# Kernel optimization log

Measured on AMD Instinct MI355X. Metric: run time of the kernel, lower is better.

## Reference

```python
import jax, jax.numpy as jnp
import numpy as np

B, C, H, W, K = 64, 64, 32, 32, 1024  # C == dim_dict, K == size_dict
BETA = 0.25


def setup_inputs() -> dict:
    key = jax.random.key(0)
    k1, k2, k3 = jax.random.split(key, 3)
    return {
        "z_from_encoder": jax.random.normal(k1, (B, C, H, W), dtype=jnp.float32),
        "codebook": jax.random.normal(k2, (K, C), dtype=jnp.float32),
        "codebook_weight": jax.random.normal(k3, (K,), dtype=jnp.float32),
        "flg_train": 1,
    }


def reference(z_from_encoder, codebook, codebook_weight, flg_train):
    # NCHW -> NHWC, flatten to (N, D)
    z = jnp.transpose(z_from_encoder, (0, 2, 3, 1))
    zf = z.reshape(-1, z.shape[-1])                      # (N, D)
    # squared euclidean distances via expansion (N, K)
    d = (jnp.sum(zf ** 2, axis=1, keepdims=True)
         + jnp.sum(codebook ** 2, axis=1)
         - 2.0 * zf @ codebook.T)
    idx = jnp.argmin(d, axis=1)                          # (N,)
    # one-hot @ codebook == gather
    z_q = codebook[idx].reshape(z.shape)                 # (B, H, W, D)
    if flg_train:
        loss = (BETA * jnp.mean((jax.lax.stop_gradient(z_q) - z) ** 2)
                + jnp.mean((z_q - jax.lax.stop_gradient(z)) ** 2))
    else:
        loss = jnp.float32(0.0)
    # straight-through estimator
    z_q_st = z + jax.lax.stop_gradient(z_q - z)
    # codebook usage histogram -> perplexity
    n_tok = zf.shape[0]
    e_mean = jnp.zeros((codebook.shape[0],), z.dtype).at[idx].add(1.0) / n_tok
    perplexity = jnp.exp(-jnp.sum(e_mean * jnp.log(e_mean + 1e-10)))
    z_q_out = jnp.transpose(z_q_st, (0, 3, 1, 2))        # back to NCHW
    return z_q_out, loss, perplexity
```

## Files before the change

kernel.cpp:

```cpp
#include <hip/hip_runtime.h>


typedef __attribute__((ext_vector_type(8))) short short8;
typedef __attribute__((ext_vector_type(4))) float float4v;

#define NELEM 4194304

#define WS_CBF   0
#define WS_C2H   262144
#define WS_HIST  266240
#define WS_LOSS  270336
#define WS_IDX   270592

__device__ __forceinline__ unsigned bf16_rne(float x) {
    unsigned u = __float_as_uint(x);
    return (u + 0x7fffu + ((u >> 16) & 1u)) >> 16;
}

__global__ __launch_bounds__(256) void prep_kernel(
    const float* __restrict__ cb, ushort* __restrict__ cbf,
    float* __restrict__ c2h, int* __restrict__ hist, float* __restrict__ loss_part) {
    __shared__ float s_c2[2][16];
    int tid  = threadIdx.x;
    int lane = tid & 63, wave = tid >> 6;
    int quad = lane >> 4, col = lane & 15;
    int bx   = blockIdx.x;

    if (bx >= 64) {
        hist[(bx - 64) * 256 + tid] = 0;
        if (bx == 64 && tid < 64) loss_part[tid] = 0.f;
        return;
    }
    int c = bx, fid = wave;
    int st = fid & 1, split = fid >> 1;
    int code  = c * 16 + col;
    int dbase = st * 32 + quad * 8;
    const float* cp = cb + code * 64 + dbase;
    float4v v0 = *(const float4v*)cp;
    float4v v1 = *(const float4v*)(cp + 4);
    float xs[8] = {v0.x, v0.y, v0.z, v0.w, v1.x, v1.y, v1.z, v1.w};
    short8 frag;
    float ssq = 0.f;
#pragma unroll
    for (int j = 0; j < 8; j++) {
        float x = xs[j];
        ssq = fmaf(x, x, ssq);
        unsigned hb = bf16_rne(x);
        if (split == 0) frag[j] = (short)hb;
        else            frag[j] = (short)bf16_rne(x - __uint_as_float(hb << 16));
    }
    *(short8*)(cbf + ((c * 4 + fid) * 64 + lane) * 8) = frag;
    if (split == 0) {
        ssq += __shfl_xor(ssq, 16);
        ssq += __shfl_xor(ssq, 32);
        if (quad == 0) s_c2[st][col] = ssq;
    }
    __syncthreads();
    if (tid < 16) c2h[c * 16 + tid] = -0.5f * (s_c2[0][tid] + s_c2[1][tid]);
}

__global__ __launch_bounds__(256, 3) void argmin_kernel(
    const float* __restrict__ z, const ushort* __restrict__ cbf,
    const float* __restrict__ c2h, int* __restrict__ idx_out, int* __restrict__ hist)
{
    __shared__ float s_ms[4][64];
    __shared__ int   s_mi[4][64];

    int tid  = threadIdx.x;
    int lane = tid & 63, wave = tid >> 6;
    int quad = lane >> 4, col = lane & 15;
    int bx   = blockIdx.x;

    int tokbase = bx * 64;
    int bb = tokbase >> 10, hwb = tokbase & 1023;
    const float* zb = z + bb * 65536 + hwb;

    short8 ah[4][2], al[4][2];
#pragma unroll
    for (int g = 0; g < 4; g++) {
        int rel = g * 16 + col;
#pragma unroll
        for (int st = 0; st < 2; st++) {
            short8 h8, l8;
#pragma unroll
            for (int j = 0; j < 8; j++) {
                int d = st * 32 + quad * 8 + j;
                float x = zb[d * 1024 + rel];
                unsigned hb = bf16_rne(x);
                h8[j] = (short)hb;
                l8[j] = (short)bf16_rne(x - __uint_as_float(hb << 16));
            }
            ah[g][st] = h8; al[g][st] = l8;
        }
    }

    float best[4][4]; int bidx[4][4];
#pragma unroll
    for (int g = 0; g < 4; g++)
#pragma unroll
        for (int r = 0; r < 4; r++) { best[g][r] = -1e38f; bidx[g][r] = 0; }

    int cbase = wave << 4;
    const ushort* cw = cbf + lane * 8;
    {
        const ushort* p0 = cw + cbase * 2048;
        short8 nb0 = *(const short8*)(p0 + 0);
        short8 nb1 = *(const short8*)(p0 + 512);
        short8 nb2 = *(const short8*)(p0 + 1024);
        short8 nb3 = *(const short8*)(p0 + 1536);
        float  nini = c2h[cbase * 16 + col];
        for (int cc = 0; cc < 16; cc++) {
            short8 bh0 = nb0, bh1 = nb1, bl0 = nb2, bl1 = nb3;
            float  ini = nini;
            if (cc < 15) {
                const ushort* np = cw + (cbase + cc + 1) * 2048;
                nb0 = *(const short8*)(np + 0);
                nb1 = *(const short8*)(np + 512);
                nb2 = *(const short8*)(np + 1024);
                nb3 = *(const short8*)(np + 1536);
                nini = c2h[(cbase + cc + 1) * 16 + col];
            }
            int code = (cbase + cc) * 16 + col;
#pragma unroll
            for (int g = 0; g < 4; g++) {
                float4v acc = {ini, ini, ini, ini};
                acc = __builtin_amdgcn_mfma_f32_16x16x32_bf16(ah[g][0], bh0, acc, 0, 0, 0);
                acc = __builtin_amdgcn_mfma_f32_16x16x32_bf16(ah[g][1], bh1, acc, 0, 0, 0);
                acc = __builtin_amdgcn_mfma_f32_16x16x32_bf16(ah[g][0], bl0, acc, 0, 0, 0);
                acc = __builtin_amdgcn_mfma_f32_16x16x32_bf16(ah[g][1], bl1, acc, 0, 0, 0);
                acc = __builtin_amdgcn_mfma_f32_16x16x32_bf16(al[g][0], bh0, acc, 0, 0, 0);
                acc = __builtin_amdgcn_mfma_f32_16x16x32_bf16(al[g][1], bh1, acc, 0, 0, 0);
#pragma unroll
                for (int r = 0; r < 4; r++) {
                    if (acc[r] > best[g][r]) { best[g][r] = acc[r]; bidx[g][r] = code; }
                }
            }
        }
    }

#pragma unroll
    for (int g = 0; g < 4; g++) {
#pragma unroll
        for (int r = 0; r < 4; r++) {
            float s = best[g][r]; int ix = bidx[g][r];
#pragma unroll
            for (int m = 1; m <= 8; m <<= 1) {
                float so = __shfl_xor(s, m);
                int   io = __shfl_xor(ix, m);
                if (so > s || (so == s && io < ix)) { s = so; ix = io; }
            }
            if (col == 0) {
                int t = g * 16 + quad * 4 + r;
                s_ms[wave][t] = s; s_mi[wave][t] = ix;
            }
        }
    }
    __syncthreads();

    if (tid < 64) {
        float sb = s_ms[0][tid]; int ib = s_mi[0][tid];
#pragma unroll
        for (int q = 1; q < 4; q++) {
            float sq_ = s_ms[q][tid];
            if (sq_ > sb) { sb = sq_; ib = s_mi[q][tid]; }
        }
        idx_out[tokbase + tid] = ib;
        atomicAdd(&hist[ib], 1);
    }
}

__global__ __launch_bounds__(256) void output_kernel(
    const float* __restrict__ z, const float* __restrict__ cb,
    const int* __restrict__ idx, float* __restrict__ out,
    float* __restrict__ loss_part)
{
    __shared__ float s_red[4];
    int tid = threadIdx.x;
    int i   = blockIdx.x * 256 + tid;
    int e0  = i * 4;
    int hw0 = e0 & 1023;
    int t   = e0 >> 10;
    int c   = t & 63, b = t >> 6;

    int4   iv = *(const int4*)(idx + b * 1024 + hw0);
    float4 zv = *(const float4*)(z + e0);
    float q0 = cb[iv.x * 64 + c];
    float q1 = cb[iv.y * 64 + c];
    float q2 = cb[iv.z * 64 + c];
    float q3 = cb[iv.w * 64 + c];
    float d0 = q0 - zv.x, d1 = q1 - zv.y, d2 = q2 - zv.z, d3 = q3 - zv.w;
    float4 ov = {zv.x + d0, zv.y + d1, zv.z + d2, zv.w + d3};
    *(float4*)(((float*)out) + e0) = ov;

    float ls = (d0 * d0 + d1 * d1) + (d2 * d2 + d3 * d3);
#pragma unroll
    for (int off = 32; off; off >>= 1) ls += __shfl_down(ls, off);
    if ((tid & 63) == 0) s_red[tid >> 6] = ls;
    __syncthreads();
    if (tid == 0) {
        float v = (s_red[0] + s_red[1]) + (s_red[2] + s_red[3]);
        atomicAdd(&loss_part[blockIdx.x & 63], v);
    }
}

__global__ __launch_bounds__(1024) void finalize_kernel(
    const int* __restrict__ hist, const float* __restrict__ loss_part,
    const int* __restrict__ flg, float* __restrict__ out) {
    __shared__ float red[16];
    int   k = threadIdx.x;
    float e = (float)hist[k] * (1.0f / 65536.0f);
    float v = e * logf(e + 1e-10f);
#pragma unroll
    for (int off = 32; off; off >>= 1) v += __shfl_down(v, off);
    if ((k & 63) == 0) red[k >> 6] = v;
    __syncthreads();
    if (k == 0) {
        float s = 0.f;
#pragma unroll
        for (int i = 0; i < 16; i++) s += red[i];
        out[NELEM + 1] = expf(-s);

        float ls = 0.f;
        for (int i = 0; i < 64; i++) ls += loss_part[i];
        float m    = ls * (1.0f / (float)NELEM);
        out[NELEM] = (*flg) ? (0.25f * m + m) : 0.0f;
    }
}

extern "C" void kernel_launch(void* const* d_in, const int* in_sizes, int n_in,
                              void* d_out, int out_size, void* d_ws, size_t ws_size,
                              hipStream_t stream) {
    const float* z   = (const float*)d_in[0];
    const float* cb  = (const float*)d_in[1];
    const int*   flg = (const int*)d_in[3];

    float* out = (float*)d_out;
    char*  ws  = (char*)d_ws;

    ushort* cbf       = (ushort*)(ws + WS_CBF);
    float*  c2h       = (float*)(ws + WS_C2H);
    int*    hist      = (int*)(ws + WS_HIST);
    float*  loss_part = (float*)(ws + WS_LOSS);
    int*    idx       = (int*)(ws + WS_IDX);

    prep_kernel<<<68, 256, 0, stream>>>(cb, cbf, c2h, hist, loss_part);
    argmin_kernel<<<1024, 256, 0, stream>>>(z, cbf, c2h, idx, hist);
    output_kernel<<<4096, 256, 0, stream>>>(z, cb, idx, out, loss_part);
    finalize_kernel<<<1, 1024, 0, stream>>>(hist, loss_part, flg, out);
}
```

Before: 150.0 us.

## Pre-split z to bf16 fragments in prep; tile output gather through LDS

The prep kernel now also converts z into hi/lo bf16 MFMA fragments and stores them in a fragment-ordered scratch buffer. That buffer lives in the output buffer, which the output kernel overwrites later. The argmin kernel then loads those fragments with coalesced vector loads instead of strided fp32 loads plus conversion. The output kernel is restructured to handle 128 tokens per block: it gathers the codebook rows into padded LDS once, then streams z and writes the output with coalesced float4 accesses. This adds an extra write and read of 16 MB of fragment data, and it depends on the output buffer being free until the output kernel runs.

```diff
diff --git a/kernel.cpp b/kernel.cpp
--- a/kernel.cpp
+++ b/kernel.cpp
@@ -17,21 +17,48 @@
     return (u + 0x7fffu + ((u >> 16) & 1u)) >> 16;
 }
 
+
 __global__ __launch_bounds__(256) void prep_kernel(
-    const float* __restrict__ cb, ushort* __restrict__ cbf,
-    float* __restrict__ c2h, int* __restrict__ hist, float* __restrict__ loss_part) {
+    const float* __restrict__ z, const float* __restrict__ cb,
+    ushort* __restrict__ zs, ushort* __restrict__ cbf, float* __restrict__ c2h,
+    int* __restrict__ hist, float* __restrict__ loss_part)
+{
     __shared__ float s_c2[2][16];
     int tid  = threadIdx.x;
     int lane = tid & 63, wave = tid >> 6;
     int quad = lane >> 4, col = lane & 15;
     int bx   = blockIdx.x;
 
-    if (bx >= 64) {
-        hist[(bx - 64) * 256 + tid] = 0;
-        if (bx == 64 && tid < 64) loss_part[tid] = 0.f;
+    if (bx < 1024) {
+        int tokbase = bx * 64;
+        int bb = tokbase >> 10, hwb = tokbase & 1023;
+        const float* zb = z + bb * 65536 + hwb;
+        int g  = wave;
+        int gg = bx * 4 + g;
+        int rel = g * 16 + col;
+#pragma unroll
+        for (int st = 0; st < 2; st++) {
+            short8 h8, l8;
+#pragma unroll
+            for (int j = 0; j < 8; j++) {
+                int d = st * 32 + quad * 8 + j;
+                float x = zb[d * 1024 + rel];
+                unsigned hb = bf16_rne(x);
+                h8[j] = (short)hb;
+                l8[j] = (short)bf16_rne(x - __uint_as_float(hb << 16));
+            }
+            int base = (((gg * 2 + st) * 4 + quad) * 2 + 0) * 16 + col;
+            *(short8*)(zs + base * 8)             = h8;
+            *(short8*)(zs + (base + 16) * 8)      = l8;
+        }
         return;
     }
-    int c = bx, fid = wave;
+    if (bx >= 1088) {
+        hist[(bx - 1088) * 256 + tid] = 0;
+        if (bx == 1088 && tid < 64) loss_part[tid] = 0.f;
+        return;
+    }
+    int c = bx - 1024, fid = wave;
     int st = fid & 1, split = fid >> 1;
     int code  = c * 16 + col;
     int dbase = st * 32 + quad * 8;
@@ -60,7 +87,7 @@
 }
 
 __global__ __launch_bounds__(256, 3) void argmin_kernel(
-    const float* __restrict__ z, const ushort* __restrict__ cbf,
+    const ushort* __restrict__ zs, const ushort* __restrict__ cbf,
     const float* __restrict__ c2h, int* __restrict__ idx_out, int* __restrict__ hist)
 {
     __shared__ float s_ms[4][64];
@@ -70,27 +97,17 @@
     int lane = tid & 63, wave = tid >> 6;
     int quad = lane >> 4, col = lane & 15;
     int bx   = blockIdx.x;
-
     int tokbase = bx * 64;
-    int bb = tokbase >> 10, hwb = tokbase & 1023;
-    const float* zb = z + bb * 65536 + hwb;
 
     short8 ah[4][2], al[4][2];
 #pragma unroll
     for (int g = 0; g < 4; g++) {
-        int rel = g * 16 + col;
+        int gg = bx * 4 + g;
 #pragma unroll
         for (int st = 0; st < 2; st++) {
-            short8 h8, l8;
-#pragma unroll
-            for (int j = 0; j < 8; j++) {
-                int d = st * 32 + quad * 8 + j;
-                float x = zb[d * 1024 + rel];
-                unsigned hb = bf16_rne(x);
-                h8[j] = (short)hb;
-                l8[j] = (short)bf16_rne(x - __uint_as_float(hb << 16));
-            }
-            ah[g][st] = h8; al[g][st] = l8;
+            int base = (((gg * 2 + st) * 4 + quad) * 2 + 0) * 16 + col;
+            ah[g][st] = *(const short8*)(zs + base * 8);
+            al[g][st] = *(const short8*)(zs + (base + 16) * 8);
         }
     }
 
@@ -174,32 +191,47 @@
     const int* __restrict__ idx, float* __restrict__ out,
     float* __restrict__ loss_part)
 {
-    __shared__ float s_red[4];
-    int tid = threadIdx.x;
-    int i   = blockIdx.x * 256 + tid;
-    int e0  = i * 4;
-    int hw0 = e0 & 1023;
-    int t   = e0 >> 10;
-    int c   = t & 63, b = t >> 6;
-
-    int4   iv = *(const int4*)(idx + b * 1024 + hw0);
-    float4 zv = *(const float4*)(z + e0);
-    float q0 = cb[iv.x * 64 + c];
-    float q1 = cb[iv.y * 64 + c];
-    float q2 = cb[iv.z * 64 + c];
-    float q3 = cb[iv.w * 64 + c];
-    float d0 = q0 - zv.x, d1 = q1 - zv.y, d2 = q2 - zv.z, d3 = q3 - zv.w;
-    float4 ov = {zv.x + d0, zv.y + d1, zv.z + d2, zv.w + d3};
-    *(float4*)(((float*)out) + e0) = ov;
-
-    float ls = (d0 * d0 + d1 * d1) + (d2 * d2 + d3 * d3);
+    __shared__ int    s_row[128];
+    __shared__ float4 s_q4[64 * 33];
+    __shared__ float  s_red[4];
+
+    int tid = threadIdx.x, bx = blockIdx.x;
+    int tokbase = bx * 128;
+    int bb = tokbase >> 10, hwb = tokbase & 1023;
+
+    if (tid < 128) s_row[tid] = idx[tokbase + tid];
+    __syncthreads();
+
+#pragma unroll
+    for (int p = 0; p < 32; p++) {
+        int i = p * 256 + tid;
+        int t = i >> 6, d = i & 63;
+        float v = cb[s_row[t] * 64 + d];
+        ((float*)s_q4)[(d * 33 + (t >> 2)) * 4 + (t & 3)] = v;
+    }
+    __syncthreads();
+
+    const float* zb = z   + bb * 65536 + hwb;
+    float*       ob = out + bb * 65536 + hwb;
+    float ls = 0.f;
+#pragma unroll
+    for (int p = 0; p < 8; p++) {
+        int fi = p * 256 + tid;
+        int d = fi >> 5, tq = fi & 31;
+        float4 zv = *(const float4*)(zb + d * 1024 + tq * 4);
+        float4 qv = s_q4[d * 33 + tq];
+        float d0 = qv.x - zv.x, d1 = qv.y - zv.y, d2 = qv.z - zv.z, d3 = qv.w - zv.w;
+        float4 ov = {zv.x + d0, zv.y + d1, zv.z + d2, zv.w + d3};
+        *(float4*)(ob + d * 1024 + tq * 4) = ov;
+        ls += (d0 * d0 + d1 * d1) + (d2 * d2 + d3 * d3);
+    }
 #pragma unroll
     for (int off = 32; off; off >>= 1) ls += __shfl_down(ls, off);
     if ((tid & 63) == 0) s_red[tid >> 6] = ls;
     __syncthreads();
     if (tid == 0) {
         float v = (s_red[0] + s_red[1]) + (s_red[2] + s_red[3]);
-        atomicAdd(&loss_part[blockIdx.x & 63], v);
+        atomicAdd(&loss_part[bx & 63], v);
     }
 }
 
@@ -242,9 +274,10 @@
     int*    hist      = (int*)(ws + WS_HIST);
     float*  loss_part = (float*)(ws + WS_LOSS);
     int*    idx       = (int*)(ws + WS_IDX);
-
-    prep_kernel<<<68, 256, 0, stream>>>(cb, cbf, c2h, hist, loss_part);
-    argmin_kernel<<<1024, 256, 0, stream>>>(z, cbf, c2h, idx, hist);
-    output_kernel<<<4096, 256, 0, stream>>>(z, cb, idx, out, loss_part);
+    ushort* zs        = (ushort*)d_out;
+
+    prep_kernel<<<1092, 256, 0, stream>>>(z, cb, zs, cbf, c2h, hist, loss_part);
+    argmin_kernel<<<1024, 256, 0, stream>>>(zs, cbf, c2h, idx, hist);
+    output_kernel<<<512, 256, 0, stream>>>(z, cb, idx, out, loss_part);
     finalize_kernel<<<1, 1024, 0, stream>>>(hist, loss_part, flg, out);
 }
```

Result: faster. 135.6 us (-9.6%).
